# Kernel tuning notes

Hardware: AMD Instinct MI355X
Metric: run time of the kernel (lower is better)

Reference implementation:

```python
import jax, jax.numpy as jnp
import numpy as np

N = 100000   # nodes
D = 128      # feature dim (inputLayerSize)
E = 600000   # edges per edge set
S = 2        # numEdgeSets
A = 1        # numAttentionLayers
PASSES = 1
OUT = 2      # outputLayerSize
HID = 80


def setup_inputs() -> dict:
    key = jax.random.key(0)
    ks = jax.random.split(key, 12)
    return {
        "nodes": jax.random.normal(ks[0], (N, D), dtype=jnp.float32),
        "edges": jax.random.randint(ks[1], (S, E, 2), 0, N),
        "problem_type": jax.random.normal(ks[2], (1, 1), dtype=jnp.float32),
        "W": jax.random.normal(ks[3], (S, D, D), dtype=jnp.float32) * 0.05,
        "att_w": jax.random.normal(ks[4], (A, 1, 2 * D), dtype=jnp.float32) * 0.05,
        "att_b": jnp.zeros((A, 1), dtype=jnp.float32),
        "fc1_w": jax.random.normal(ks[5], (HID, D + 1), dtype=jnp.float32) * 0.05,
        "fc1_b": jnp.zeros((HID,), dtype=jnp.float32),
        "fc2_w": jax.random.normal(ks[6], (HID, HID), dtype=jnp.float32) * 0.05,
        "fc2_b": jnp.zeros((HID,), dtype=jnp.float32),
        "fc3_w": jax.random.normal(ks[7], (OUT, HID), dtype=jnp.float32) * 0.05,
        "fc3_b": jnp.zeros((OUT,), dtype=jnp.float32),
    }


def _segment_softmax(e, dst, n):
    # e: [E,1] logits, dst: [E] segment ids -> softmax within each dst group
    m = jax.ops.segment_max(e, dst, num_segments=n)          # [N,1]
    ex = jnp.exp(e - m[dst])                                 # [E,1]
    s = jax.ops.segment_sum(ex, dst, num_segments=n)         # [N,1]
    return ex / s[dst]


def reference(nodes, edges, problem_type, W, att_w, att_b,
              fc1_w, fc1_b, fc2_w, fc2_b, fc3_w, fc3_b):
    h = nodes
    for _ in range(PASSES):
        h_prime = jnp.zeros_like(h)
        for s in range(S):
            src = edges[s, :, 0]
            dst = edges[s, :, 1]
            for a in range(A):
                h_i = h[src] @ W[s]                          # [E,D]
                h_j = h[dst] @ W[s]                          # [E,D]
                logits = jnp.concatenate([h_i, h_j], axis=1) @ att_w[a].T + att_b[a]
                e = jax.nn.leaky_relu(logits)                # [E,1]
                alpha = _segment_softmax(e, dst, N)          # [E,1]
                h_prime = h_prime.at[src].add(alpha * h_j)   # scatter-add to src
            # original divides cumulative hPrime after each edge set
            h_prime = h_prime / A
        h = h_prime
    g = h.mean(axis=0)                                       # [D] graph readout
    x = jnp.concatenate([g[None, :], problem_type], axis=1)  # [1, D+1]
    x = jax.nn.leaky_relu(x @ fc1_w.T + fc1_b)
    x = jax.nn.leaky_relu(x @ fc2_w.T + fc2_b)
    return x @ fc3_w.T + fc3_b                               # [1, OUT]
```

## Files before the change

### kernel.cpp

```cpp
#include <hip/hip_runtime.h>
#include <stdint.h>


#define NN   100000
#define DD   128
#define EE   600000
#define SS   2
#define HIDN 80

__device__ __forceinline__ float leaky(float x) { return x > 0.f ? x : 0.01f * x; }

__global__ __launch_bounds__(256) void k_flags(const int2* __restrict__ e2,
                                               uint8_t* __restrict__ flags) {
    int i = blockIdx.x * 256 + threadIdx.x;
    if (i < SS * EE) {
        int dst = e2[i].y;
        int s   = (i >= EE) ? 1 : 0;
        flags[s * NN + dst] = 1;
    }
}

__global__ __launch_bounds__(256) void k_msum(const float4* __restrict__ nodes4,
                                              const uint8_t* __restrict__ flags,
                                              float* __restrict__ sums) {
    const int cq = threadIdx.x & 31;
    const int rg = threadIdx.x >> 5;
    float4 a0 = {0.f, 0.f, 0.f, 0.f};
    float4 a1 = {0.f, 0.f, 0.f, 0.f};
    const int stride = gridDim.x * 8;
    for (int n = blockIdx.x * 8 + rg; n < NN; n += stride) {
        float4 v = nodes4[n * 32 + cq];
        float m0 = flags[n]      ? 1.f : 0.f;
        float m1 = flags[NN + n] ? 1.f : 0.f;
        a0.x = fmaf(v.x, m0, a0.x); a0.y = fmaf(v.y, m0, a0.y);
        a0.z = fmaf(v.z, m0, a0.z); a0.w = fmaf(v.w, m0, a0.w);
        a1.x = fmaf(v.x, m1, a1.x); a1.y = fmaf(v.y, m1, a1.y);
        a1.z = fmaf(v.z, m1, a1.z); a1.w = fmaf(v.w, m1, a1.w);
    }
    __shared__ float sh[256];
    sh[threadIdx.x] = 0.f;
    __syncthreads();
    atomicAdd(&sh[4 * cq + 0],       a0.x);
    atomicAdd(&sh[4 * cq + 1],       a0.y);
    atomicAdd(&sh[4 * cq + 2],       a0.z);
    atomicAdd(&sh[4 * cq + 3],       a0.w);
    atomicAdd(&sh[128 + 4 * cq + 0], a1.x);
    atomicAdd(&sh[128 + 4 * cq + 1], a1.y);
    atomicAdd(&sh[128 + 4 * cq + 2], a1.z);
    atomicAdd(&sh[128 + 4 * cq + 3], a1.w);
    __syncthreads();
    atomicAdd(&sums[threadIdx.x], sh[threadIdx.x]);
}

__global__ __launch_bounds__(128) void k_final(const float* __restrict__ sums,
                                               const float* __restrict__ W,
                                               const float* __restrict__ pt,
                                               const float* __restrict__ fc1w,
                                               const float* __restrict__ fc1b,
                                               const float* __restrict__ fc2w,
                                               const float* __restrict__ fc2b,
                                               const float* __restrict__ fc3w,
                                               const float* __restrict__ fc3b,
                                               float* __restrict__ out) {
    __shared__ float s0[DD], s1[DD], x[DD + 4], y1[HIDN], y2[HIDN];
    const int t = threadIdx.x;
    s0[t] = sums[t];
    s1[t] = sums[DD + t];
    __syncthreads();
    float g = 0.f;
    #pragma unroll 4
    for (int k = 0; k < DD; ++k) {
        g = fmaf(s0[k], W[k * DD + t], g);
        g = fmaf(s1[k], W[DD * DD + k * DD + t], g);
    }
    x[t] = g * (1.0f / (float)NN);
    if (t == 0) x[DD] = pt[0];
    __syncthreads();
    if (t < HIDN) {
        float acc = fc1b[t];
        #pragma unroll 4
        for (int j = 0; j < DD + 1; ++j) acc = fmaf(x[j], fc1w[t * (DD + 1) + j], acc);
        y1[t] = leaky(acc);
    }
    __syncthreads();
    if (t < HIDN) {
        float acc = fc2b[t];
        #pragma unroll 4
        for (int j = 0; j < HIDN; ++j) acc = fmaf(y1[j], fc2w[t * HIDN + j], acc);
        y2[t] = leaky(acc);
    }
    __syncthreads();
    if (t < 2) {
        float acc = fc3b[t];
        for (int j = 0; j < HIDN; ++j) acc = fmaf(y2[j], fc3w[t * HIDN + j], acc);
        out[t] = acc;
    }
}

extern "C" void kernel_launch(void* const* d_in, const int* in_sizes, int n_in,
                              void* d_out, int out_size, void* d_ws, size_t ws_size,
                              hipStream_t stream) {
    const float4* nodes4 = (const float4*)d_in[0];
    const int2*   edges  = (const int2*)d_in[1];
    const float*  pt     = (const float*)d_in[2];
    const float*  W      = (const float*)d_in[3];
    const float*  fc1w   = (const float*)d_in[6];
    const float*  fc1b   = (const float*)d_in[7];
    const float*  fc2w   = (const float*)d_in[8];
    const float*  fc2b   = (const float*)d_in[9];
    const float*  fc3w   = (const float*)d_in[10];
    const float*  fc3b   = (const float*)d_in[11];
    float* out = (float*)d_out;

    float*   sums  = (float*)d_ws;
    uint8_t* flags = (uint8_t*)d_ws + 1024;

    hipMemsetAsync(d_ws, 0, 1024 + (size_t)SS * NN, stream);
    k_flags<<<(SS * EE + 255) / 256, 256, 0, stream>>>(edges, flags);
    k_msum<<<512, 256, 0, stream>>>(nodes4, flags, sums);
    k_final<<<1, 128, 0, stream>>>(sums, W, pt, fc1w, fc1b, fc2w, fc2b,
                                   fc3w, fc3b, out);
}
```

Baseline: 158.7 us.

## Vectorize edge flag loads, unroll masked sum, spread atomics, widen final kernel

The flag kernel now reads two edges per thread with int4 loads. The masked node sum runs on 1024 blocks, keeps two rows in flight per iteration, and spreads its global atomics over 8 partial-sum copies to reduce contention. The final MLP kernel uses 1024 threads to split the W projection across 8 chunks and stages the fc weights in shared memory. In exchange it adds extra reduction steps and uses much more shared memory in a single-block kernel.

```diff
diff --git a/kernel.cpp b/kernel.cpp
--- a/kernel.cpp
+++ b/kernel.cpp
@@ -7,35 +7,49 @@
 #define EE   600000
 #define SS   2
 #define HIDN 80
+#define MS_BLOCKS 1024
 
 __device__ __forceinline__ float leaky(float x) { return x > 0.f ? x : 0.01f * x; }
 
-__global__ __launch_bounds__(256) void k_flags(const int2* __restrict__ e2,
+__global__ __launch_bounds__(256) void k_flags(const int4* __restrict__ e4,
                                                uint8_t* __restrict__ flags) {
     int i = blockIdx.x * 256 + threadIdx.x;
-    if (i < SS * EE) {
-        int dst = e2[i].y;
-        int s   = (i >= EE) ? 1 : 0;
-        flags[s * NN + dst] = 1;
+    if (i < SS * EE / 2) {
+        int4 v = e4[i];
+        int s = (i >= EE / 2) ? 1 : 0;
+        flags[s * NN + v.y] = 1;
+        flags[s * NN + v.w] = 1;
     }
 }
 
 __global__ __launch_bounds__(256) void k_msum(const float4* __restrict__ nodes4,
                                               const uint8_t* __restrict__ flags,
-                                              float* __restrict__ sums) {
+                                              float* __restrict__ sums8) {
     const int cq = threadIdx.x & 31;
     const int rg = threadIdx.x >> 5;
     float4 a0 = {0.f, 0.f, 0.f, 0.f};
     float4 a1 = {0.f, 0.f, 0.f, 0.f};
-    const int stride = gridDim.x * 8;
-    for (int n = blockIdx.x * 8 + rg; n < NN; n += stride) {
+    const int stride = MS_BLOCKS * 8;
+    for (int n = blockIdx.x * 8 + rg; n < NN; n += 2 * stride) {
         float4 v = nodes4[n * 32 + cq];
         float m0 = flags[n]      ? 1.f : 0.f;
         float m1 = flags[NN + n] ? 1.f : 0.f;
+        int n2 = n + stride;
+        float4 v2 = {0.f, 0.f, 0.f, 0.f};
+        float p0 = 0.f, p1 = 0.f;
+        if (n2 < NN) {
+            v2 = nodes4[n2 * 32 + cq];
+            p0 = flags[n2]      ? 1.f : 0.f;
+            p1 = flags[NN + n2] ? 1.f : 0.f;
+        }
         a0.x = fmaf(v.x, m0, a0.x); a0.y = fmaf(v.y, m0, a0.y);
         a0.z = fmaf(v.z, m0, a0.z); a0.w = fmaf(v.w, m0, a0.w);
         a1.x = fmaf(v.x, m1, a1.x); a1.y = fmaf(v.y, m1, a1.y);
         a1.z = fmaf(v.z, m1, a1.z); a1.w = fmaf(v.w, m1, a1.w);
+        a0.x = fmaf(v2.x, p0, a0.x); a0.y = fmaf(v2.y, p0, a0.y);
+        a0.z = fmaf(v2.z, p0, a0.z); a0.w = fmaf(v2.w, p0, a0.w);
+        a1.x = fmaf(v2.x, p1, a1.x); a1.y = fmaf(v2.y, p1, a1.y);
+        a1.z = fmaf(v2.z, p1, a1.z); a1.w = fmaf(v2.w, p1, a1.w);
     }
     __shared__ float sh[256];
     sh[threadIdx.x] = 0.f;
@@ -49,51 +63,87 @@
     atomicAdd(&sh[128 + 4 * cq + 2], a1.z);
     atomicAdd(&sh[128 + 4 * cq + 3], a1.w);
     __syncthreads();
-    atomicAdd(&sums[threadIdx.x], sh[threadIdx.x]);
+    atomicAdd(&sums8[(blockIdx.x & 7) * 256 + threadIdx.x], sh[threadIdx.x]);
 }
 
-__global__ __launch_bounds__(128) void k_final(const float* __restrict__ sums,
-                                               const float* __restrict__ W,
-                                               const float* __restrict__ pt,
-                                               const float* __restrict__ fc1w,
-                                               const float* __restrict__ fc1b,
-                                               const float* __restrict__ fc2w,
-                                               const float* __restrict__ fc2b,
-                                               const float* __restrict__ fc3w,
-                                               const float* __restrict__ fc3b,
-                                               float* __restrict__ out) {
-    __shared__ float s0[DD], s1[DD], x[DD + 4], y1[HIDN], y2[HIDN];
-    const int t = threadIdx.x;
-    s0[t] = sums[t];
-    s1[t] = sums[DD + t];
+__global__ __launch_bounds__(1024) void k_final(const float* __restrict__ sums8,
+                                                const float* __restrict__ W,
+                                                const float* __restrict__ pt,
+                                                const float* __restrict__ fc1w,
+                                                const float* __restrict__ fc1b,
+                                                const float* __restrict__ fc2w,
+                                                const float* __restrict__ fc2b,
+                                                const float* __restrict__ fc3w,
+                                                const float* __restrict__ fc3b,
+                                                float* __restrict__ out) {
+    __shared__ float s01[2 * DD];
+    __shared__ float fc1w_s[HIDN * 129];
+    __shared__ float fc2w_s[HIDN * 81];
+    __shared__ float fc3w_s[2 * HIDN];
+    __shared__ float fc1b_s[HIDN], fc2b_s[HIDN], fc3b_s[2];
+    __shared__ float part[8][DD];
+    __shared__ float x[DD + 4], y1[HIDN], y2[HIDN];
+
+    const int tid = threadIdx.x;
+    const int c = tid >> 7;
+    const int t = tid & 127;
+
+    if (tid < 256) {
+        float s = 0.f;
+        #pragma unroll
+        for (int r = 0; r < 8; ++r) s += sums8[r * 256 + tid];
+        s01[tid] = s;
+    }
+    float w0[16], w1[16];
+    #pragma unroll
+    for (int k = 0; k < 16; ++k) {
+        w0[k] = W[(c * 16 + k) * DD + t];
+        w1[k] = W[DD * DD + (c * 16 + k) * DD + t];
+    }
+    for (int i = tid; i < HIDN * 129; i += 1024) fc1w_s[i] = fc1w[i];
+    for (int i = tid; i < HIDN * HIDN; i += 1024)
+        fc2w_s[(i / HIDN) * 81 + (i % HIDN)] = fc2w[i];
+    if (tid < 2 * HIDN) fc3w_s[tid] = fc3w[tid];
+    if (tid >= 512 && tid < 512 + HIDN) fc1b_s[tid - 512] = fc1b[tid - 512];
+    if (tid >= 640 && tid < 640 + HIDN) fc2b_s[tid - 640] = fc2b[tid - 640];
+    if (tid >= 768 && tid < 770) fc3b_s[tid - 768] = fc3b[tid - 768];
+    float ptv = (tid == 1023) ? pt[0] : 0.f;
     __syncthreads();
-    float g = 0.f;
-    #pragma unroll 4
-    for (int k = 0; k < DD; ++k) {
-        g = fmaf(s0[k], W[k * DD + t], g);
-        g = fmaf(s1[k], W[DD * DD + k * DD + t], g);
+
+    float p = 0.f;
+    #pragma unroll
+    for (int k = 0; k < 16; ++k)
+        p = fmaf(s01[c * 16 + k], w0[k], fmaf(s01[DD + c * 16 + k], w1[k], p));
+    part[c][t] = p;
+    __syncthreads();
+
+    if (tid < DD) {
+        float g = 0.f;
+        #pragma unroll
+        for (int cc = 0; cc < 8; ++cc) g += part[cc][tid];
+        x[tid] = g * (1.0f / (float)NN);
     }
-    x[t] = g * (1.0f / (float)NN);
-    if (t == 0) x[DD] = pt[0];
+    if (tid == 1023) x[DD] = ptv;
     __syncthreads();
-    if (t < HIDN) {
-        float acc = fc1b[t];
+
+    if (tid < HIDN) {
+        float acc = fc1b_s[tid];
         #pragma unroll 4
-        for (int j = 0; j < DD + 1; ++j) acc = fmaf(x[j], fc1w[t * (DD + 1) + j], acc);
-        y1[t] = leaky(acc);
+        for (int j = 0; j < DD + 1; ++j) acc = fmaf(x[j], fc1w_s[tid * 129 + j], acc);
+        y1[tid] = leaky(acc);
     }
     __syncthreads();
-    if (t < HIDN) {
-        float acc = fc2b[t];
+    if (tid < HIDN) {
+        float acc = fc2b_s[tid];
         #pragma unroll 4
-        for (int j = 0; j < HIDN; ++j) acc = fmaf(y1[j], fc2w[t * HIDN + j], acc);
-        y2[t] = leaky(acc);
+        for (int j = 0; j < HIDN; ++j) acc = fmaf(y1[j], fc2w_s[tid * 81 + j], acc);
+        y2[tid] = leaky(acc);
     }
     __syncthreads();
-    if (t < 2) {
-        float acc = fc3b[t];
-        for (int j = 0; j < HIDN; ++j) acc = fmaf(y2[j], fc3w[t * HIDN + j], acc);
-        out[t] = acc;
+    if (tid < 2) {
+        float acc = fc3b_s[tid];
+        for (int j = 0; j < HIDN; ++j) acc = fmaf(y2[j], fc3w_s[tid * HIDN + j], acc);
+        out[tid] = acc;
     }
 }
 
@@ -101,7 +151,7 @@
                               void* d_out, int out_size, void* d_ws, size_t ws_size,
                               hipStream_t stream) {
     const float4* nodes4 = (const float4*)d_in[0];
-    const int2*   edges  = (const int2*)d_in[1];
+    const int4*   edges  = (const int4*)d_in[1];
     const float*  pt     = (const float*)d_in[2];
     const float*  W      = (const float*)d_in[3];
     const float*  fc1w   = (const float*)d_in[6];
@@ -112,12 +162,12 @@
     const float*  fc3b   = (const float*)d_in[11];
     float* out = (float*)d_out;
 
-    float*   sums  = (float*)d_ws;
-    uint8_t* flags = (uint8_t*)d_ws + 1024;
+    float*   sums8 = (float*)d_ws;
+    uint8_t* flags = (uint8_t*)d_ws + 8192;
 
-    hipMemsetAsync(d_ws, 0, 1024 + (size_t)SS * NN, stream);
-    k_flags<<<(SS * EE + 255) / 256, 256, 0, stream>>>(edges, flags);
-    k_msum<<<512, 256, 0, stream>>>(nodes4, flags, sums);
-    k_final<<<1, 128, 0, stream>>>(sums, W, pt, fc1w, fc1b, fc2w, fc2b,
-                                   fc3w, fc3b, out);
+    hipMemsetAsync(d_ws, 0, 8192 + (size_t)SS * NN, stream);
+    k_flags<<<(SS * EE / 2 + 255) / 256, 256, 0, stream>>>(edges, flags);
+    k_msum<<<MS_BLOCKS, 256, 0, stream>>>(nodes4, flags, sums8);
+    k_final<<<1, 1024, 0, stream>>>(sums8, W, pt, fc1w, fc1b, fc2w, fc2b,
+                                    fc3w, fc3b, out);
 }
```

New measurement: 136.3 us. 1.16x faster.
